# Kernel tuning notes

Measured on AMD Instinct MI355X. Metric: run time of the kernel, lower is better.

## Reference

```python
import jax, jax.numpy as jnp
import numpy as np

IN_DIMS = 256
EMBED_DIMS = 512
NUM_HEADS = 8
GRID = 16  # forced: arrange2 hardcodes 256 = GRID*GRID tokens
HEAD_DIM = EMBED_DIMS // NUM_HEADS
LN_EPS = 1e-5


def setup_inputs() -> dict:
    key = jax.random.key(0)
    ks = jax.random.split(key, 12)
    B = 8
    s_in = 1.0 / np.sqrt(IN_DIMS)
    s_emb = 1.0 / np.sqrt(EMBED_DIMS)
    return {
        "x1": jax.random.normal(ks[0], (B, IN_DIMS, GRID, GRID), jnp.float32),
        "x2": jax.random.normal(ks[1], (B, IN_DIMS, GRID, GRID), jnp.float32),
        # 1x1 conv weights stored as [out, in]
        "Wq": jax.random.normal(ks[2], (EMBED_DIMS, IN_DIMS), jnp.float32) * s_in,
        "bq": jnp.zeros((EMBED_DIMS,), jnp.float32),
        "Wk": jax.random.normal(ks[3], (EMBED_DIMS, IN_DIMS), jnp.float32) * s_in,
        "bk": jnp.zeros((EMBED_DIMS,), jnp.float32),
        "Wv": jax.random.normal(ks[4], (EMBED_DIMS, IN_DIMS), jnp.float32) * s_in,
        "bv": jnp.zeros((EMBED_DIMS,), jnp.float32),
        "Wa": jax.random.normal(ks[5], (IN_DIMS, EMBED_DIMS), jnp.float32) * s_emb,
        "ba": jnp.zeros((IN_DIMS,), jnp.float32),
        "ln_g": jnp.ones((IN_DIMS,), jnp.float32),
        "ln_b": jnp.zeros((IN_DIMS,), jnp.float32),
        "Wl": jax.random.normal(ks[6], (IN_DIMS, IN_DIMS), jnp.float32) * s_in,
        "bl": jnp.zeros((IN_DIMS,), jnp.float32),
    }


def _conv1x1(x, W, b):
    # x: [b, Cin, h, w]; W: [Cout, Cin]
    return jnp.einsum('bihw,oi->bohw', x, W) + b[None, :, None, None]


def _arrange(t):
    # 'b (c head) h w -> head b (h w) c'  (c outer, head inner in channel axis)
    b = t.shape[0]
    t = t.reshape(b, HEAD_DIM, NUM_HEADS, GRID * GRID)
    return t.transpose(2, 0, 3, 1)  # [head, b, n, c]


def reference(x1, x2, Wq, bq, Wk, bk, Wv, bv, Wa, ba, ln_g, ln_b, Wl, bl):
    B, Cin, H, W = x1.shape
    N = H * W  # 256
    q = _arrange(_conv1x1(x1, Wq, bq))                     # [h, b, n, c]
    k = _arrange(_conv1x1(x2, Wk, bk))                     # [h, q, m, c]
    v = _arrange(_conv1x1(x2, Wv, bv)).reshape(NUM_HEADS, B * N, HEAD_DIM)  # [h, (b m), c]
    # cross-batch attention logits (NOTE: original never applies self.scale)
    attn = jnp.einsum('pbnc,pqmc->pbqnm', q, k)            # [h, b, q, n, m]
    attn = jax.nn.softmax(attn, axis=-1)
    # 'head b q n m -> b head n (q m)'
    attn = attn.transpose(1, 0, 3, 2, 4).reshape(B, NUM_HEADS, N, B * N)
    out = jnp.einsum('bhnm,hmc->bhnc', attn, v)            # [b, h, n, c]
    # 'b head (h w) c -> b (c head) h w'
    out = out.transpose(0, 3, 1, 2).reshape(B, EMBED_DIMS, H, W)
    a = _conv1x1(out, Wa, ba) + x1                          # residual, [b, Cin, h, w]
    # proj_out: rearrange -> LayerNorm -> Linear -> ReLU -> rearrange back
    t = a.reshape(B, Cin, N).transpose(0, 2, 1)            # [b, n, Cin]
    mu = t.mean(-1, keepdims=True)
    var = ((t - mu) ** 2).mean(-1, keepdims=True)
    t = (t - mu) * jax.lax.rsqrt(var + LN_EPS) * ln_g + ln_b
    t = jax.nn.relu(t @ Wl.T + bl)
    return t.transpose(0, 2, 1).reshape(B, Cin, H, W)
```

## Files before the change

kernel.cpp:

```cpp
#include <hip/hip_runtime.h>

typedef unsigned short u16;
typedef unsigned int   u32;
typedef __attribute__((ext_vector_type(8))) short bf16x8;
typedef __attribute__((ext_vector_type(4))) float f32x4;

#define BB   8
#define CIN  256
#define NT   256
#define EMB  512
#define NH   8

__device__ __forceinline__ float bf2f(u16 b) {
    union { u32 u; float f; } v; v.u = ((u32)b) << 16; return v.f;
}
__device__ __forceinline__ u16 f2bf(float f) {
    union { float f; u32 u; } v; v.f = f;
    u32 r = v.u + 0x7FFFu + ((v.u >> 16) & 1u);
    return (u16)(r >> 16);
}
__device__ __forceinline__ float ld(const u16* base, size_t idx, int f32) {
    return f32 ? ((const float*)base)[idx] : bf2f(base[idx]);
}

struct alignas(16) U32x4 { u32 x, y, z, w; };

#define FMA44(AP, S, A4, B4) do { \
  (AP)[0*(S)+0] += (A4).x*(B4).x; (AP)[0*(S)+1] += (A4).x*(B4).y; (AP)[0*(S)+2] += (A4).x*(B4).z; (AP)[0*(S)+3] += (A4).x*(B4).w; \
  (AP)[1*(S)+0] += (A4).y*(B4).x; (AP)[1*(S)+1] += (A4).y*(B4).y; (AP)[1*(S)+2] += (A4).y*(B4).z; (AP)[1*(S)+3] += (A4).y*(B4).w; \
  (AP)[2*(S)+0] += (A4).z*(B4).x; (AP)[2*(S)+1] += (A4).z*(B4).y; (AP)[2*(S)+2] += (A4).z*(B4).z; (AP)[2*(S)+3] += (A4).z*(B4).w; \
  (AP)[3*(S)+0] += (A4).w*(B4).x; (AP)[3*(S)+1] += (A4).w*(B4).y; (AP)[3*(S)+2] += (A4).w*(B4).z; (AP)[3*(S)+3] += (A4).w*(B4).w; \
} while (0)

__global__ void k_detect(const u16* __restrict__ x1, int* __restrict__ flag) {
    __shared__ int cnt;
    if (threadIdx.x == 0) cnt = 0;
    __syncthreads();
    int t = threadIdx.x;
    int local = 0;
    for (int j = t * 16; j < t * 16 + 16; j += 2) {
        u16 w = x1[j];
        int e = (w >> 7) & 0xFF;
        if (e >= 100 && e <= 145) local++;
    }
    atomicAdd(&cnt, local);
    __syncthreads();
    if (t == 0) *flag = (cnt >= 1200) ? 0 : 1;
}

__global__ void k_qkv(
    const u16* __restrict__ x1, const u16* __restrict__ x2,
    const u16* __restrict__ Wq, const u16* __restrict__ bq,
    const u16* __restrict__ Wk, const u16* __restrict__ bk,
    const u16* __restrict__ Wv, const u16* __restrict__ bv,
    u16* __restrict__ Qg, u16* __restrict__ Kg, u16* __restrict__ Vg,
    const int* __restrict__ flag)
{
    const int f32 = *flag;
    int id = blockIdx.x;
    int proj = id >> 8;
    int rem  = id & 255;
    int b  = rem >> 5;
    int ot = (rem >> 2) & 7;
    int nt = rem & 3;

    const u16* X    = (proj == 0) ? x1 : x2;
    const u16* W    = (proj == 0) ? Wq : (proj == 1) ? Wk : Wv;
    const u16* bias = (proj == 0) ? bq : (proj == 1) ? bk : bv;

    __shared__ float Ws[64][68];
    __shared__ float Xs[64][64];

    int t = threadIdx.x;
    int lane64 = t & 63;
    int quad   = t >> 6;
    int og = t >> 4;
    int ng = t & 15;

    float acc[16];
#pragma unroll
    for (int j = 0; j < 16; ++j) acc[j] = 0.f;

    float wreg[16], xreg[16];
#pragma unroll
    for (int p = 0; p < 16; ++p) {
        int o = quad + 4*p;
        wreg[p] = ld(W, (size_t)(ot*64 + o)*CIN + 0*64 + lane64, f32);
    }
#pragma unroll
    for (int p = 0; p < 16; ++p) {
        int i = quad + 4*p;
        xreg[p] = ld(X, ((size_t)b*CIN + 0*64 + i)*NT + nt*64 + lane64, f32);
    }

    for (int kc = 0; kc < 4; ++kc) {
        __syncthreads();
#pragma unroll
        for (int p = 0; p < 16; ++p)
            Ws[lane64][quad + 4*p] = wreg[p];
#pragma unroll
        for (int p = 0; p < 16; ++p)
            Xs[quad + 4*p][lane64] = xreg[p];
        __syncthreads();

        if (kc < 3) {
            int kn = kc + 1;
#pragma unroll
            for (int p = 0; p < 16; ++p) {
                int o = quad + 4*p;
                wreg[p] = ld(W, (size_t)(ot*64 + o)*CIN + kn*64 + lane64, f32);
            }
#pragma unroll
            for (int p = 0; p < 16; ++p) {
                int i = quad + 4*p;
                xreg[p] = ld(X, ((size_t)b*CIN + kn*64 + i)*NT + nt*64 + lane64, f32);
            }
        }

#pragma unroll 8
        for (int i = 0; i < 64; ++i) {
            float4 w4 = *(const float4*)&Ws[i][og*4];
            float4 x4 = *(const float4*)&Xs[i][ng*4];
            FMA44(acc, 4, w4, x4);
        }
    }
    __syncthreads();

#pragma unroll
    for (int jo = 0; jo < 4; ++jo) {
        int o = ot*64 + og*4 + jo;
        float bb = ld(bias, o, f32);
#pragma unroll
        for (int jn = 0; jn < 4; ++jn)
            Ws[og*4 + jo][ng*4 + jn] = acc[jo*4 + jn] + bb;
    }
    __syncthreads();

    if (proj < 2) {
        u16* OUT = (proj == 0) ? Qg : Kg;
        int hh = t >> 5;
        int nb = t & 31;
#pragma unroll
        for (int p = 0; p < 2; ++p) {
            int nn = nb + 32*p;
            u32 pk[4];
#pragma unroll
            for (int e = 0; e < 4; ++e) {
                u16 lo = f2bf(Ws[(2*e  )*8 + hh][nn]);
                u16 hi = f2bf(Ws[(2*e+1)*8 + hh][nn]);
                pk[e] = (u32)lo | ((u32)hi << 16);
            }
            U32x4 v; v.x = pk[0]; v.y = pk[1]; v.z = pk[2]; v.w = pk[3];
            *(U32x4*)&OUT[((size_t)((hh*8 + b)*256) + nt*64 + nn)*64 + ot*8] = v;
        }
    } else {
        int rr = t >> 2;
        int hh = rr & 7, cl = rr >> 3;
        int nq = t & 3;
        u32 pk[8];
#pragma unroll
        for (int e = 0; e < 8; ++e) {
            u16 lo = f2bf(Ws[cl*8 + hh][nq*16 + 2*e  ]);
            u16 hi = f2bf(Ws[cl*8 + hh][nq*16 + 2*e+1]);
            pk[e] = (u32)lo | ((u32)hi << 16);
        }
        size_t base = ((size_t)((hh*8 + b)*64) + ot*8 + cl)*256 + nt*64 + nq*16;
        U32x4 v0; v0.x = pk[0]; v0.y = pk[1]; v0.z = pk[2]; v0.w = pk[3];
        U32x4 v1; v1.x = pk[4]; v1.y = pk[5]; v1.z = pk[6]; v1.w = pk[7];
        *(U32x4*)&Vg[base]     = v0;
        *(U32x4*)&Vg[base + 8] = v1;
    }
}

__global__ __launch_bounds__(256) void k_attn(
    const u16* __restrict__ Qg, const u16* __restrict__ Kg,
    const u16* __restrict__ Vg, float* __restrict__ Oph)
{
    int bid = blockIdx.x;
    int h   = bid >> 6;
    int kbg = (bid >> 5) & 1;
    int b   = (bid >> 2) & 7;
    int ntq = bid & 3;

    int t = threadIdx.x;
    int l = t & 63, w = t >> 6;
    int quad = l >> 4, col = l & 15;

    __shared__ __align__(16) u16 S[16384];

    int q = ntq*64 + w*16 + col;
    const size_t qrow = ((size_t)(h*8 + b)*256 + q)*64;
    bf16x8 qf0 = *(const bf16x8*)&Qg[qrow +  0 + quad*8];
    bf16x8 qf1 = *(const bf16x8*)&Qg[qrow + 32 + quad*8];

    const int lswz2 = l ^ (((l >> 4) & 1) << 1);
    const int lswz4 = l ^ (((l >> 4) & 1) << 2);

    f32x4 Oacc[4];
#pragma unroll
    for (int ct = 0; ct < 4; ++ct) { Oacc[ct][0]=0.f; Oacc[ct][1]=0.f; Oacc[ct][2]=0.f; Oacc[ct][3]=0.f; }

    for (int kb2 = 0; kb2 < 4; ++kb2) {
        int kb = kbg*4 + kb2;
        __syncthreads();
        const size_t kbase = (size_t)(h*8 + kb) * 256 * 64;
#pragma unroll
        for (int i = 0; i < 8; ++i) {
            int g = i*256 + t;
            int key = g >> 3, cc = g & 7;
            int tt = key >> 4, klo = key & 15, kc = cc >> 2, qs = cc & 3;
            int pos = qs*16 + (klo ^ ((qs & 1) << 1) ^ (kc << 2));
            U32x4 v = *(const U32x4*)&Kg[kbase + (size_t)key*64 + cc*8];
            *(U32x4*)&S[(size_t)(((tt*2 + kc)*64) + pos)*8] = v;
        }
        __syncthreads();

        f32x4 Sfr[16];
#pragma unroll
        for (int tt = 0; tt < 16; ++tt) { Sfr[tt][0]=0.f; Sfr[tt][1]=0.f; Sfr[tt][2]=0.f; Sfr[tt][3]=0.f; }
#pragma unroll
        for (int tt = 0; tt < 16; ++tt) {
            bf16x8 k0 = *(const bf16x8*)&S[(size_t)((tt*2 + 0)*64 + lswz2)*8];
            bf16x8 k1 = *(const bf16x8*)&S[(size_t)((tt*2 + 1)*64 + (lswz2 ^ 4))*8];
            Sfr[tt] = __builtin_amdgcn_mfma_f32_16x16x32_bf16(k0, qf0, Sfr[tt], 0, 0, 0);
            Sfr[tt] = __builtin_amdgcn_mfma_f32_16x16x32_bf16(k1, qf1, Sfr[tt], 0, 0, 0);
        }

        float inv;
        {
            float m = Sfr[0][0];
#pragma unroll
            for (int tt = 0; tt < 16; ++tt)
#pragma unroll
                for (int r = 0; r < 4; ++r) m = fmaxf(m, Sfr[tt][r]);
            m = fmaxf(m, __shfl_xor(m, 16));
            m = fmaxf(m, __shfl_xor(m, 32));
            float s = 0.f;
#pragma unroll
            for (int tt = 0; tt < 16; ++tt)
#pragma unroll
                for (int r = 0; r < 4; ++r) {
                    float e = __expf(Sfr[tt][r] - m);
                    Sfr[tt][r] = e; s += e;
                }
            s += __shfl_xor(s, 16);
            s += __shfl_xor(s, 32);
            inv = 1.f / s;
        }

        bf16x8 pf[8];
#pragma unroll
        for (int ch = 0; ch < 8; ++ch) {
            float a0 = Sfr[2*ch  ][0]*inv, a1 = Sfr[2*ch  ][1]*inv;
            float a2 = Sfr[2*ch  ][2]*inv, a3 = Sfr[2*ch  ][3]*inv;
            float b0 = Sfr[2*ch+1][0]*inv, b1 = Sfr[2*ch+1][1]*inv;
            float b2 = Sfr[2*ch+1][2]*inv, b3 = Sfr[2*ch+1][3]*inv;
            u32 u0, u1, v0, v1;
            asm("v_cvt_pk_bf16_f32 %0, %1, %2" : "=v"(u0) : "v"(a0), "v"(a1));
            asm("v_cvt_pk_bf16_f32 %0, %1, %2" : "=v"(u1) : "v"(a2), "v"(a3));
            asm("v_cvt_pk_bf16_f32 %0, %1, %2" : "=v"(v0) : "v"(b0), "v"(b1));
            asm("v_cvt_pk_bf16_f32 %0, %1, %2" : "=v"(v1) : "v"(b2), "v"(b3));
            asm("v_permlane32_swap_b32 %0, %1" : "+v"(u0), "+v"(v0));
            asm("v_permlane16_swap_b32 %0, %1" : "+v"(u0), "+v"(v0));
            asm("v_permlane32_swap_b32 %0, %1" : "+v"(u1), "+v"(v1));
            asm("v_permlane16_swap_b32 %0, %1" : "+v"(u1), "+v"(v1));
            union { u32 wd[4]; bf16x8 hB; } pu;
            pu.wd[0] = u0; pu.wd[1] = u1; pu.wd[2] = v0; pu.wd[3] = v1;
            pf[ch] = pu.hB;
        }
        __syncthreads();

        const size_t vbase = (size_t)(h*8 + kb) * 64 * 256;
#pragma unroll
        for (int i = 0; i < 8; ++i) {
            int g = i*256 + t;
            int cg = g >> 5, k16 = g & 31;
            int ct = cg >> 4, clo = cg & 15, ch = k16 >> 2, qs = k16 & 3;
            int pos = (qs*16 + clo) ^ ch ^ ((qs & 1) << 2);
            U32x4 v = *(const U32x4*)&Vg[vbase + (size_t)cg*256 + k16*8];
            *(U32x4*)&S[(size_t)(((ch*4 + ct)*64) + pos)*8] = v;
        }
        __syncthreads();

#pragma unroll
        for (int ch = 0; ch < 8; ++ch)
#pragma unroll
            for (int ct = 0; ct < 4; ++ct) {
                bf16x8 vb = *(const bf16x8*)&S[(size_t)(((ch*4 + ct)*64) + (lswz4 ^ ch))*8];
                Oacc[ct] = __builtin_amdgcn_mfma_f32_16x16x32_bf16(pf[ch], vb, Oacc[ct], 0, 0, 0);
            }
    }

    const size_t obase = (size_t)(h*8 + b) * 256 * 64;
    int n0 = ntq*64 + w*16 + quad*4;
#pragma unroll
    for (int ct = 0; ct < 4; ++ct)
#pragma unroll
        for (int r = 0; r < 4; ++r)
            atomicAdd(&Oph[obase + (size_t)(n0 + r)*64 + ct*16 + col], Oacc[ct][r]);
}

__global__ void k_proj_res(
    const float* __restrict__ Oph, const u16* __restrict__ Wa,
    const u16* __restrict__ ba, const u16* __restrict__ x1,
    float* __restrict__ Ap, const int* __restrict__ flag)
{
    const int f32 = *flag;
    int id = blockIdx.x;
    int tt = id >> 2;
    int it = id & 3;
    int tok0 = tt * 32;
    int b  = tok0 >> 8;
    int n0 = tok0 & 255;

    __shared__ float Was[64][68];
    __shared__ float Os[64][36];

    int t = threadIdx.x;
    int lane64 = t & 63, quad = t >> 6;
    int ig = t & 15;
    int tg = t >> 4;

    int tk = t & 31;
    int hh = t >> 5;

    float wreg[16];
    float oreg[8];

    {
#pragma unroll
        for (int p = 0; p < 16; ++p) {
            int i = quad + 4*p;
            wreg[p] = ld(Wa, (size_t)(it*64 + i)*EMB + 0*64 + lane64, f32);
        }
        const float* src = &Oph[(((size_t)(hh*8 + b))*256 + n0 + tk)*64 + 0*8];
        float4 v0 = *(const float4*)&src[0];
        float4 v1 = *(const float4*)&src[4];
        oreg[0]=v0.x; oreg[1]=v0.y; oreg[2]=v0.z; oreg[3]=v0.w;
        oreg[4]=v1.x; oreg[5]=v1.y; oreg[6]=v1.z; oreg[7]=v1.w;
    }

    float acc[8];
#pragma unroll
    for (int j = 0; j < 8; ++j) acc[j] = 0.f;

    for (int kc = 0; kc < 8; ++kc) {
        __syncthreads();
#pragma unroll
        for (int p = 0; p < 16; ++p)
            Was[lane64][quad + 4*p] = wreg[p];
#pragma unroll
        for (int e = 0; e < 8; ++e)
            Os[e*8 + hh][tk] = oreg[e];
        __syncthreads();

        if (kc < 7) {
            int kn = kc + 1;
#pragma unroll
            for (int p = 0; p < 16; ++p) {
                int i = quad + 4*p;
                wreg[p] = ld(Wa, (size_t)(it*64 + i)*EMB + kn*64 + lane64, f32);
            }
            const float* src = &Oph[(((size_t)(hh*8 + b))*256 + n0 + tk)*64 + kn*8];
            float4 v0 = *(const float4*)&src[0];
            float4 v1 = *(const float4*)&src[4];
            oreg[0]=v0.x; oreg[1]=v0.y; oreg[2]=v0.z; oreg[3]=v0.w;
            oreg[4]=v1.x; oreg[5]=v1.y; oreg[6]=v1.z; oreg[7]=v1.w;
        }

#pragma unroll 8
        for (int o = 0; o < 64; ++o) {
            float4 w4 = *(const float4*)&Was[o][ig*4];
            float2 t2 = *(const float2*)&Os[o][tg*2];
            acc[0] += w4.x*t2.x; acc[1] += w4.y*t2.x;
            acc[2] += w4.z*t2.x; acc[3] += w4.w*t2.x;
            acc[4] += w4.x*t2.y; acc[5] += w4.y*t2.y;
            acc[6] += w4.z*t2.y; acc[7] += w4.w*t2.y;
        }
    }

    int i0 = it*64 + ig*4;
    float ba0 = ld(ba, i0+0, f32), ba1 = ld(ba, i0+1, f32);
    float ba2 = ld(ba, i0+2, f32), ba3 = ld(ba, i0+3, f32);
#pragma unroll
    for (int jt = 0; jt < 2; ++jt) {
        int token = tok0 + tg*2 + jt;
        int n = n0 + tg*2 + jt;
        float4 v;
        v.x = acc[jt*4+0] + ba0 + ld(x1, ((size_t)b*CIN + i0+0)*NT + n, f32);
        v.y = acc[jt*4+1] + ba1 + ld(x1, ((size_t)b*CIN + i0+1)*NT + n, f32);
        v.z = acc[jt*4+2] + ba2 + ld(x1, ((size_t)b*CIN + i0+2)*NT + n, f32);
        v.w = acc[jt*4+3] + ba3 + ld(x1, ((size_t)b*CIN + i0+3)*NT + n, f32);
        *(float4*)&Ap[(size_t)token*CIN + i0] = v;
    }
}

__global__ void k_ln_out(
    const float* __restrict__ Ap, const u16* __restrict__ ln_g,
    const u16* __restrict__ ln_b, const u16* __restrict__ Wl,
    const u16* __restrict__ bl, u16* __restrict__ out,
    const int* __restrict__ flag)
{
    const int f32 = *flag;
    int tok0 = blockIdx.x * 8;
    int b  = tok0 >> 8;
    int n0 = tok0 & 255;

    __shared__ float At[8][260];

    int t = threadIdx.x;
#pragma unroll
    for (int k = 0; k < 8; ++k)
        At[k][t] = Ap[((size_t)tok0 + k)*CIN + t];
    __syncthreads();

    {
        int kk = t >> 5, lme = t & 31;
        float s = 0.f, s2 = 0.f;
#pragma unroll
        for (int ii = 0; ii < 8; ++ii) { float v = At[kk][lme + 32*ii]; s += v; s2 += v*v; }
#pragma unroll
        for (int off = 1; off < 32; off <<= 1) { s += __shfl_xor(s, off); s2 += __shfl_xor(s2, off); }
        float mu   = s  * (1.f/256.f);
        float var  = s2 * (1.f/256.f) - mu*mu;
        float rstd = rsqrtf(var + 1e-5f);
#pragma unroll
        for (int ii = 0; ii < 8; ++ii) {
            int i = lme + 32*ii;
            float v = At[kk][i];
            At[kk][i] = (v - mu) * rstd * ld(ln_g, i, f32) + ld(ln_b, i, f32);
        }
    }
    __syncthreads();

    int j = t;
    float acc[8];
#pragma unroll
    for (int k = 0; k < 8; ++k) acc[k] = 0.f;

    if (f32) {
        const float* wrow = (const float*)Wl + (size_t)j*CIN;
#pragma unroll 2
        for (int i4 = 0; i4 < 64; ++i4) {
            float4 w4 = *(const float4*)&wrow[4*i4];
#pragma unroll
            for (int k = 0; k < 8; ++k) {
                float4 a = *(const float4*)&At[k][4*i4];
                acc[k] += w4.x*a.x + w4.y*a.y + w4.z*a.z + w4.w*a.w;
            }
        }
    } else {
        const u32* wrow = (const u32*)(Wl + (size_t)j*CIN);
#pragma unroll 2
        for (int i4 = 0; i4 < 64; ++i4) {
            u32 w01 = wrow[2*i4+0], w23 = wrow[2*i4+1];
            float c0 = bf2f((u16)(w01 & 0xFFFFu)), c1 = bf2f((u16)(w01 >> 16));
            float c2 = bf2f((u16)(w23 & 0xFFFFu)), c3 = bf2f((u16)(w23 >> 16));
#pragma unroll
            for (int k = 0; k < 8; ++k) {
                float4 a = *(const float4*)&At[k][4*i4];
                acc[k] += c0*a.x + c1*a.y + c2*a.z + c3*a.w;
            }
        }
    }

    float blv = ld(bl, j, f32);
    size_t obase = ((size_t)b*CIN + j)*NT + n0;
    if (f32) {
        float* o32 = (float*)out;
#pragma unroll
        for (int k = 0; k < 8; ++k)
            o32[obase + k] = fmaxf(acc[k] + blv, 0.f);
    } else {
        u32 pk[4];
#pragma unroll
        for (int k = 0; k < 4; ++k) {
            float f0 = fmaxf(acc[2*k+0] + blv, 0.f);
            float f1 = fmaxf(acc[2*k+1] + blv, 0.f);
            pk[k] = (u32)f2bf(f0) | ((u32)f2bf(f1) << 16);
        }
        U32x4 a0; a0.x = pk[0]; a0.y = pk[1]; a0.z = pk[2]; a0.w = pk[3];
        *(U32x4*)(out + obase) = a0;
    }
}

extern "C" void kernel_launch(void* const* d_in, const int* in_sizes, int n_in,
                              void* d_out, int out_size, void* d_ws, size_t ws_size,
                              hipStream_t stream)
{
    const u16* x1   = (const u16*)d_in[0];
    const u16* x2   = (const u16*)d_in[1];
    const u16* Wq   = (const u16*)d_in[2];
    const u16* bq   = (const u16*)d_in[3];
    const u16* Wk   = (const u16*)d_in[4];
    const u16* bk   = (const u16*)d_in[5];
    const u16* Wv   = (const u16*)d_in[6];
    const u16* bv   = (const u16*)d_in[7];
    const u16* Wa   = (const u16*)d_in[8];
    const u16* ba   = (const u16*)d_in[9];
    const u16* ln_g = (const u16*)d_in[10];
    const u16* ln_b = (const u16*)d_in[11];
    const u16* Wl   = (const u16*)d_in[12];
    const u16* bl   = (const u16*)d_in[13];
    u16* out = (u16*)d_out;

    int* flag = (int*)d_ws;
    u16* Qg = (u16*)d_ws + 32;
    u16* Kg = Qg + (size_t)BB*EMB*NT;
    u16* Vg = Kg + (size_t)BB*EMB*NT;
    float* Oph = (float*)(Vg + (size_t)BB*EMB*NT);
    float* Ap  = Oph + (size_t)BB*EMB*NT;

    hipMemsetAsync(Oph, 0, (size_t)BB*EMB*NT*sizeof(float), stream);

    k_detect  <<<1,   256, 0, stream>>>(x1, flag);
    k_qkv     <<<768, 256, 0, stream>>>(x1, x2, Wq, bq, Wk, bk, Wv, bv, Qg, Kg, Vg, flag);
    k_attn    <<<512, 256, 0, stream>>>(Qg, Kg, Vg, Oph);
    k_proj_res<<<256, 256, 0, stream>>>(Oph, Wa, ba, x1, Ap, flag);
    k_ln_out  <<<256, 256, 0, stream>>>(Ap, ln_g, ln_b, Wl, bl, out, flag);
}
```

Measured before the change: 187.3 us.

## Move QKV projection to split-bf16 MFMA and replace attention atomics with slabs

Adds a pre-pass that transposes inputs and weights into hi/lo bf16 pairs. The QKV 1x1 convolutions then run on bf16 MFMA instructions using three products (hi*hi, lo*hi, hi*lo) to keep close to fp32 accuracy, replacing the scalar FP32 FMA tiling. Attention now writes each key-batch-group partial to its own slab instead of using atomicAdd, so the memset disappears and proj_res sums the two slabs on load. The cost is an extra kernel launch, more workspace, and extra memory traffic for the split copies.

```diff
diff --git a/kernel.cpp b/kernel.cpp
--- a/kernel.cpp
+++ b/kernel.cpp
@@ -48,11 +48,94 @@
     if (t == 0) *flag = (cnt >= 1200) ? 0 : 1;
 }
 
-__global__ void k_qkv(
+__global__ void k_xpose(
     const u16* __restrict__ x1, const u16* __restrict__ x2,
-    const u16* __restrict__ Wq, const u16* __restrict__ bq,
-    const u16* __restrict__ Wk, const u16* __restrict__ bk,
-    const u16* __restrict__ Wv, const u16* __restrict__ bv,
+    const u16* __restrict__ Wq, const u16* __restrict__ Wk, const u16* __restrict__ Wv,
+    u16* __restrict__ XTh, u16* __restrict__ XTl,
+    u16* __restrict__ WCh, u16* __restrict__ WCl)
+{
+    __shared__ int cnt;
+    __shared__ float T[64][65];
+    int t = threadIdx.x;
+    if (t == 0) cnt = 0;
+    __syncthreads();
+    {
+        int local = 0;
+        for (int j = t * 16; j < t * 16 + 16; j += 2) {
+            u16 w = x1[j];
+            int e = (w >> 7) & 0xFF;
+            if (e >= 100 && e <= 145) local++;
+        }
+        atomicAdd(&cnt, local);
+    }
+    __syncthreads();
+    const int f32 = (cnt >= 1200) ? 0 : 1;
+
+    int bid = blockIdx.x;
+    if (bid < 256) {
+        int inp = bid >> 7, b = (bid >> 4) & 7, ks = (bid >> 2) & 3, ns = bid & 3;
+        const u16* X = inp ? x2 : x1;
+#pragma unroll
+        for (int p = 0; p < 4; ++p) {
+            int kk = p * 16 + (t >> 4);
+            int nn = (t & 15) * 4;
+#pragma unroll
+            for (int j = 0; j < 4; ++j)
+                T[kk][nn + j] = ld(X, ((size_t)b * CIN + ks * 64 + kk) * NT + ns * 64 + nn + j, f32);
+        }
+        __syncthreads();
+#pragma unroll
+        for (int it = 0; it < 2; ++it) {
+            int g = it * 256 + t;
+            int nn = g >> 3, kg = g & 7;
+            u32 hw[4], lw[4];
+#pragma unroll
+            for (int e = 0; e < 4; ++e) {
+                float va = T[kg * 8 + 2 * e][nn];
+                float vb = T[kg * 8 + 2 * e + 1][nn];
+                u16 ha = f2bf(va), hb = f2bf(vb);
+                u16 la = f2bf(va - bf2f(ha)), lb = f2bf(vb - bf2f(hb));
+                hw[e] = (u32)ha | ((u32)hb << 16);
+                lw[e] = (u32)la | ((u32)lb << 16);
+            }
+            size_t dst = (((size_t)(inp * 8 + b) * 256) + ns * 64 + nn) * 256 + ks * 64 + kg * 8;
+            U32x4 H; H.x = hw[0]; H.y = hw[1]; H.z = hw[2]; H.w = hw[3];
+            U32x4 L; L.x = lw[0]; L.y = lw[1]; L.z = lw[2]; L.w = lw[3];
+            *(U32x4*)&XTh[dst] = H;
+            *(U32x4*)&XTl[dst] = L;
+        }
+    } else {
+        int wb = bid - 256;
+        int proj = wb >> 2, qtr = wb & 3;
+        const u16* W = (proj == 0) ? Wq : (proj == 1) ? Wk : Wv;
+#pragma unroll
+        for (int it = 0; it < 16; ++it) {
+            int g = it * 256 + t;
+            int row = g >> 5, kg = g & 31;
+            int o = qtr * 128 + row;
+            u32 hw[4], lw[4];
+#pragma unroll
+            for (int e = 0; e < 4; ++e) {
+                float va = ld(W, (size_t)o * CIN + kg * 8 + 2 * e, f32);
+                float vb = ld(W, (size_t)o * CIN + kg * 8 + 2 * e + 1, f32);
+                u16 ha = f2bf(va), hb = f2bf(vb);
+                u16 la = f2bf(va - bf2f(ha)), lb = f2bf(vb - bf2f(hb));
+                hw[e] = (u32)ha | ((u32)hb << 16);
+                lw[e] = (u32)la | ((u32)lb << 16);
+            }
+            size_t dst = ((size_t)(proj * 512 + o)) * 256 + kg * 8;
+            U32x4 H; H.x = hw[0]; H.y = hw[1]; H.z = hw[2]; H.w = hw[3];
+            U32x4 L; L.x = lw[0]; L.y = lw[1]; L.z = lw[2]; L.w = lw[3];
+            *(U32x4*)&WCh[dst] = H;
+            *(U32x4*)&WCl[dst] = L;
+        }
+    }
+}
+
+__global__ __launch_bounds__(256) void k_qkv(
+    const u16* __restrict__ XTh, const u16* __restrict__ XTl,
+    const u16* __restrict__ WCh, const u16* __restrict__ WCl,
+    const u16* __restrict__ bq, const u16* __restrict__ bk, const u16* __restrict__ bv,
     u16* __restrict__ Qg, u16* __restrict__ Kg, u16* __restrict__ Vg,
     const int* __restrict__ flag)
 {
@@ -64,75 +147,74 @@
     int ot = (rem >> 2) & 7;
     int nt = rem & 3;
 
-    const u16* X    = (proj == 0) ? x1 : x2;
-    const u16* W    = (proj == 0) ? Wq : (proj == 1) ? Wk : Wv;
+    __shared__ __align__(16) u16 SB[16384];
+    const int WHO = 0, WLO = 4096, XHO = 8192, XLO = 12288;
+
+    int t = threadIdx.x;
+    int l = t & 63, w = t >> 6;
+    int quad = l >> 4, col = l & 15;
+    const int lswz2 = l ^ (((l >> 4) & 1) << 1);
+
+    const u16* Wh  = WCh + ((size_t)proj * 512 + ot * 64) * 256;
+    const u16* Wlo = WCl + ((size_t)proj * 512 + ot * 64) * 256;
+    int inp = (proj == 0) ? 0 : 1;
+    const u16* Xh  = XTh + (((size_t)(inp * 8 + b)) * 256 + nt * 64) * 256;
+    const u16* Xlo = XTl + (((size_t)(inp * 8 + b)) * 256 + nt * 64) * 256;
+
+    f32x4 acc[4];
+#pragma unroll
+    for (int n4 = 0; n4 < 4; ++n4) { acc[n4][0]=0.f; acc[n4][1]=0.f; acc[n4][2]=0.f; acc[n4][3]=0.f; }
+
+    for (int c4 = 0; c4 < 4; ++c4) {
+        __syncthreads();
+#pragma unroll
+        for (int it = 0; it < 2; ++it) {
+            int g = it * 256 + t;
+            int row = g >> 3, cc = g & 7;
+            int tt = row >> 4, klo = row & 15, kch = cc >> 2, qs = cc & 3;
+            int pos = qs * 16 + (klo ^ ((qs & 1) << 1) ^ (kch << 2));
+            int off = ((tt * 2 + kch) * 64 + pos) * 8;
+            size_t src = (size_t)row * 256 + c4 * 64 + cc * 8;
+            *(U32x4*)&SB[WHO + off] = *(const U32x4*)&Wh[src];
+            *(U32x4*)&SB[WLO + off] = *(const U32x4*)&Wlo[src];
+            *(U32x4*)&SB[XHO + off] = *(const U32x4*)&Xh[src];
+            *(U32x4*)&SB[XLO + off] = *(const U32x4*)&Xlo[src];
+        }
+        __syncthreads();
+
+        int sA0 = ((w * 2 + 0) * 64 + lswz2) * 8;
+        int sA1 = ((w * 2 + 1) * 64 + (lswz2 ^ 4)) * 8;
+        bf16x8 aH0 = *(const bf16x8*)&SB[WHO + sA0];
+        bf16x8 aH1 = *(const bf16x8*)&SB[WHO + sA1];
+        bf16x8 aL0 = *(const bf16x8*)&SB[WLO + sA0];
+        bf16x8 aL1 = *(const bf16x8*)&SB[WLO + sA1];
+#pragma unroll
+        for (int n4 = 0; n4 < 4; ++n4) {
+            int sB0 = ((n4 * 2 + 0) * 64 + lswz2) * 8;
+            int sB1 = ((n4 * 2 + 1) * 64 + (lswz2 ^ 4)) * 8;
+            bf16x8 bH0 = *(const bf16x8*)&SB[XHO + sB0];
+            bf16x8 bH1 = *(const bf16x8*)&SB[XHO + sB1];
+            bf16x8 bL0 = *(const bf16x8*)&SB[XLO + sB0];
+            bf16x8 bL1 = *(const bf16x8*)&SB[XLO + sB1];
+            acc[n4] = __builtin_amdgcn_mfma_f32_16x16x32_bf16(aH0, bH0, acc[n4], 0, 0, 0);
+            acc[n4] = __builtin_amdgcn_mfma_f32_16x16x32_bf16(aH1, bH1, acc[n4], 0, 0, 0);
+            acc[n4] = __builtin_amdgcn_mfma_f32_16x16x32_bf16(aL0, bH0, acc[n4], 0, 0, 0);
+            acc[n4] = __builtin_amdgcn_mfma_f32_16x16x32_bf16(aL1, bH1, acc[n4], 0, 0, 0);
+            acc[n4] = __builtin_amdgcn_mfma_f32_16x16x32_bf16(aH0, bL0, acc[n4], 0, 0, 0);
+            acc[n4] = __builtin_amdgcn_mfma_f32_16x16x32_bf16(aH1, bL1, acc[n4], 0, 0, 0);
+        }
+    }
+    __syncthreads();
+
+    float (*EP)[68] = (float (*)[68])SB;
     const u16* bias = (proj == 0) ? bq : (proj == 1) ? bk : bv;
-
-    __shared__ float Ws[64][68];
-    __shared__ float Xs[64][64];
-
-    int t = threadIdx.x;
-    int lane64 = t & 63;
-    int quad   = t >> 6;
-    int og = t >> 4;
-    int ng = t & 15;
-
-    float acc[16];
-#pragma unroll
-    for (int j = 0; j < 16; ++j) acc[j] = 0.f;
-
-    float wreg[16], xreg[16];
-#pragma unroll
-    for (int p = 0; p < 16; ++p) {
-        int o = quad + 4*p;
-        wreg[p] = ld(W, (size_t)(ot*64 + o)*CIN + 0*64 + lane64, f32);
-    }
-#pragma unroll
-    for (int p = 0; p < 16; ++p) {
-        int i = quad + 4*p;
-        xreg[p] = ld(X, ((size_t)b*CIN + 0*64 + i)*NT + nt*64 + lane64, f32);
-    }
-
-    for (int kc = 0; kc < 4; ++kc) {
-        __syncthreads();
-#pragma unroll
-        for (int p = 0; p < 16; ++p)
-            Ws[lane64][quad + 4*p] = wreg[p];
-#pragma unroll
-        for (int p = 0; p < 16; ++p)
-            Xs[quad + 4*p][lane64] = xreg[p];
-        __syncthreads();
-
-        if (kc < 3) {
-            int kn = kc + 1;
-#pragma unroll
-            for (int p = 0; p < 16; ++p) {
-                int o = quad + 4*p;
-                wreg[p] = ld(W, (size_t)(ot*64 + o)*CIN + kn*64 + lane64, f32);
-            }
-#pragma unroll
-            for (int p = 0; p < 16; ++p) {
-                int i = quad + 4*p;
-                xreg[p] = ld(X, ((size_t)b*CIN + kn*64 + i)*NT + nt*64 + lane64, f32);
-            }
-        }
-
-#pragma unroll 8
-        for (int i = 0; i < 64; ++i) {
-            float4 w4 = *(const float4*)&Ws[i][og*4];
-            float4 x4 = *(const float4*)&Xs[i][ng*4];
-            FMA44(acc, 4, w4, x4);
-        }
-    }
-    __syncthreads();
-
-#pragma unroll
-    for (int jo = 0; jo < 4; ++jo) {
-        int o = ot*64 + og*4 + jo;
-        float bb = ld(bias, o, f32);
-#pragma unroll
-        for (int jn = 0; jn < 4; ++jn)
-            Ws[og*4 + jo][ng*4 + jn] = acc[jo*4 + jn] + bb;
+#pragma unroll
+    for (int r = 0; r < 4; ++r) {
+        int ol = w * 16 + quad * 4 + r;
+        float bb = ld(bias, ot * 64 + ol, f32);
+#pragma unroll
+        for (int n4 = 0; n4 < 4; ++n4)
+            EP[ol][n4 * 16 + col] = acc[n4][r] + bb;
     }
     __syncthreads();
 
@@ -142,16 +224,16 @@
         int nb = t & 31;
 #pragma unroll
         for (int p = 0; p < 2; ++p) {
-            int nn = nb + 32*p;
+            int nn = nb + 32 * p;
             u32 pk[4];
 #pragma unroll
             for (int e = 0; e < 4; ++e) {
-                u16 lo = f2bf(Ws[(2*e  )*8 + hh][nn]);
-                u16 hi = f2bf(Ws[(2*e+1)*8 + hh][nn]);
+                u16 lo = f2bf(EP[(2 * e) * 8 + hh][nn]);
+                u16 hi = f2bf(EP[(2 * e + 1) * 8 + hh][nn]);
                 pk[e] = (u32)lo | ((u32)hi << 16);
             }
             U32x4 v; v.x = pk[0]; v.y = pk[1]; v.z = pk[2]; v.w = pk[3];
-            *(U32x4*)&OUT[((size_t)((hh*8 + b)*256) + nt*64 + nn)*64 + ot*8] = v;
+            *(U32x4*)&OUT[((size_t)((hh * 8 + b) * 256) + nt * 64 + nn) * 64 + ot * 8] = v;
         }
     } else {
         int rr = t >> 2;
@@ -160,11 +242,11 @@
         u32 pk[8];
 #pragma unroll
         for (int e = 0; e < 8; ++e) {
-            u16 lo = f2bf(Ws[cl*8 + hh][nq*16 + 2*e  ]);
-            u16 hi = f2bf(Ws[cl*8 + hh][nq*16 + 2*e+1]);
+            u16 lo = f2bf(EP[cl * 8 + hh][nq * 16 + 2 * e]);
+            u16 hi = f2bf(EP[cl * 8 + hh][nq * 16 + 2 * e + 1]);
             pk[e] = (u32)lo | ((u32)hi << 16);
         }
-        size_t base = ((size_t)((hh*8 + b)*64) + ot*8 + cl)*256 + nt*64 + nq*16;
+        size_t base = ((size_t)((hh * 8 + b) * 64) + ot * 8 + cl) * 256 + nt * 64 + nq * 16;
         U32x4 v0; v0.x = pk[0]; v0.y = pk[1]; v0.z = pk[2]; v0.w = pk[3];
         U32x4 v1; v1.x = pk[4]; v1.y = pk[5]; v1.z = pk[6]; v1.w = pk[7];
         *(U32x4*)&Vg[base]     = v0;
@@ -291,13 +373,14 @@
             }
     }
 
+    float* Op = Oph + (size_t)kbg * ((size_t)BB * EMB * NT);
     const size_t obase = (size_t)(h*8 + b) * 256 * 64;
     int n0 = ntq*64 + w*16 + quad*4;
 #pragma unroll
     for (int ct = 0; ct < 4; ++ct)
 #pragma unroll
         for (int r = 0; r < 4; ++r)
-            atomicAdd(&Oph[obase + (size_t)(n0 + r)*64 + ct*16 + col], Oacc[ct][r]);
+            Op[obase + (size_t)(n0 + r)*64 + ct*16 + col] = Oacc[ct][r];
 }
 
 __global__ void k_proj_res(
@@ -324,6 +407,8 @@
     int tk = t & 31;
     int hh = t >> 5;
 
+    const size_t SLAB = (size_t)BB * EMB * NT;
+
     float wreg[16];
     float oreg[8];
 
@@ -336,8 +421,10 @@
         const float* src = &Oph[(((size_t)(hh*8 + b))*256 + n0 + tk)*64 + 0*8];
         float4 v0 = *(const float4*)&src[0];
         float4 v1 = *(const float4*)&src[4];
-        oreg[0]=v0.x; oreg[1]=v0.y; oreg[2]=v0.z; oreg[3]=v0.w;
-        oreg[4]=v1.x; oreg[5]=v1.y; oreg[6]=v1.z; oreg[7]=v1.w;
+        float4 u0 = *(const float4*)&src[SLAB];
+        float4 u1 = *(const float4*)&src[SLAB + 4];
+        oreg[0]=v0.x+u0.x; oreg[1]=v0.y+u0.y; oreg[2]=v0.z+u0.z; oreg[3]=v0.w+u0.w;
+        oreg[4]=v1.x+u1.x; oreg[5]=v1.y+u1.y; oreg[6]=v1.z+u1.z; oreg[7]=v1.w+u1.w;
     }
 
     float acc[8];
@@ -364,8 +451,10 @@
             const float* src = &Oph[(((size_t)(hh*8 + b))*256 + n0 + tk)*64 + kn*8];
             float4 v0 = *(const float4*)&src[0];
             float4 v1 = *(const float4*)&src[4];
-            oreg[0]=v0.x; oreg[1]=v0.y; oreg[2]=v0.z; oreg[3]=v0.w;
-            oreg[4]=v1.x; oreg[5]=v1.y; oreg[6]=v1.z; oreg[7]=v1.w;
+            float4 u0 = *(const float4*)&src[SLAB];
+            float4 u1 = *(const float4*)&src[SLAB + 4];
+            oreg[0]=v0.x+u0.x; oreg[1]=v0.y+u0.y; oreg[2]=v0.z+u0.z; oreg[3]=v0.w+u0.w;
+            oreg[4]=v1.x+u1.x; oreg[5]=v1.y+u1.y; oreg[6]=v1.z+u1.z; oreg[7]=v1.w+u1.w;
         }
 
 #pragma unroll 8
@@ -509,12 +598,15 @@
     u16* Kg = Qg + (size_t)BB*EMB*NT;
     u16* Vg = Kg + (size_t)BB*EMB*NT;
     float* Oph = (float*)(Vg + (size_t)BB*EMB*NT);
-    float* Ap  = Oph + (size_t)BB*EMB*NT;
-
-    hipMemsetAsync(Oph, 0, (size_t)BB*EMB*NT*sizeof(float), stream);
+    float* Ap  = Oph + 2*(size_t)BB*EMB*NT;
+    u16* XTh = (u16*)(Ap + (size_t)BB*NT*CIN);
+    u16* XTl = XTh + (size_t)2*BB*NT*CIN;
+    u16* WCh = XTl + (size_t)2*BB*NT*CIN;
+    u16* WCl = WCh + (size_t)3*EMB*CIN;
 
     k_detect  <<<1,   256, 0, stream>>>(x1, flag);
-    k_qkv     <<<768, 256, 0, stream>>>(x1, x2, Wq, bq, Wk, bk, Wv, bv, Qg, Kg, Vg, flag);
+    k_xpose   <<<268, 256, 0, stream>>>(x1, x2, Wq, Wk, Wv, XTh, XTl, WCh, WCl);
+    k_qkv     <<<768, 256, 0, stream>>>(XTh, XTl, WCh, WCl, bq, bk, bv, Qg, Kg, Vg, flag);
     k_attn    <<<512, 256, 0, stream>>>(Qg, Kg, Vg, Oph);
     k_proj_res<<<256, 256, 0, stream>>>(Oph, Wa, ba, x1, Ap, flag);
     k_ln_out  <<<256, 256, 0, stream>>>(Ap, ln_g, ln_b, Wl, bl, out, flag);
```

Result: no change. 185.0 us (-1.2%).
